# Optimization experiments

Measured on AMD Instinct MI355X. Metric: run time of the kernel, lower is better.

Reference implementation:

```python
import jax, jax.numpy as jnp
import numpy as np
from jax import lax

EPS = 1e-5  # torch BatchNorm2d default


def setup_inputs() -> dict:
    key = jax.random.key(0)
    k1, k2 = jax.random.split(key)
    x = jax.random.normal(k1, (8, 32, 28, 28), dtype=jnp.float32)
    # AdderConv.param: [out_channel, in_channel, k, k], init ~ N(0,1)
    W = jax.random.normal(k2, (64, 32, 3, 3), dtype=jnp.float32)
    # BatchNorm2d affine params at init
    gamma = jnp.ones((64,), dtype=jnp.float32)
    beta = jnp.zeros((64,), dtype=jnp.float32)
    return {"x": x, "W": W, "gamma": gamma, "beta": beta}


def _adder(patches, Wc):
    # patches: [N, K, Ho, Wo] with K = C*kh*kw (channel-major, matching torch unfold)
    # Wc: [O, K]
    # AdderNet: out[n,o,ho,wo] = -sum_k |patches[n,k,ho,wo] - Wc[o,k]|
    diff = patches[:, None, :, :, :] - Wc[None, :, :, None, None]  # [N,O,K,Ho,Wo]
    return -jnp.abs(diff).sum(axis=2)  # [N,O,Ho,Wo]


def reference(x, W, gamma, beta):
    O, C, kh, kw = W.shape
    # im2col, same layout as torch.nn.functional.unfold: feature dim = C*kh*kw
    patches = lax.conv_general_dilated_patches(
        x, (kh, kw), window_strides=(1, 1), padding=[(1, 1), (1, 1)]
    )  # [N, C*kh*kw, Ho, Wo]
    Wc = W.reshape(O, C * kh * kw)
    out = _adder(patches, Wc)  # [N, O, Ho, Wo]
    # BatchNorm2d, training mode (batch statistics, biased variance)
    mean = out.mean(axis=(0, 2, 3), keepdims=True)
    var = out.var(axis=(0, 2, 3), keepdims=True)
    y = (out - mean) * lax.rsqrt(var + EPS)
    return y * gamma[None, :, None, None] + beta[None, :, None, None]
```

## Files before the change

### kernel.cpp

```cpp
#include <hip/hip_runtime.h>

#define NB   8
#define CIN  32
#define HH   28
#define WW   28
#define OC   64
#define HWSZ (HH*WW)
#define TOTAL (NB*OC*HWSZ)
#define CNT  (NB*HWSZ)

#define TROWS 4
#define TCOLS 32
#define TSZ  (CIN*TROWS*TCOLS)

#define CPW  2
#define CHGRP 8
#define NCOPY 32

__global__ __launch_bounds__(256) void adder_stats_kernel(
    const float* __restrict__ x, const float* __restrict__ Wt,
    float* __restrict__ raw, double* __restrict__ Sbuf)
{
    __shared__ float xs[TSZ];
    const int t     = threadIdx.x;
    const int bid   = blockIdx.x;
    const int chgrp = bid & (CHGRP-1);
    const int sp    = bid >> 3;
    const int rp    = sp % 14;
    const int n     = bid / (CHGRP * 14);
    const int h0    = rp * 2;
    const int copy  = sp & (NCOPY-1);

    for (int i = t; i < TSZ; i += 256) {
        int cc  = i >> 7;
        int r   = (i >> 5) & 3;
        int col = i & 31;
        int hh  = h0 - 1 + r;
        int ww  = col - 1;
        float v = 0.0f;
        if (hh >= 0 && hh < HH && (unsigned)ww < (unsigned)WW)
            v = x[((n*CIN + cc)*HH + hh)*WW + ww];
        xs[i] = v;
    }
    __syncthreads();

    const int lane  = t & 63;
    const int g     = __builtin_amdgcn_readfirstlane(t >> 6);
    const bool valid = lane < 56;
    const int p     = valid ? lane : 0;
    const int pr    = p / WW;
    const int pw    = p % WW;
    const int o_base = chgrp*8 + g*CPW;
    const int b0    = pr*TCOLS + pw;

    float acc[CPW];
    #pragma unroll
    for (int oo = 0; oo < CPW; ++oo) acc[oo] = 0.0f;

    for (int cc = 0; cc < CIN; ++cc) {
        float xr[9];
        #pragma unroll
        for (int dr = 0; dr < 3; ++dr)
            #pragma unroll
            for (int dc = 0; dc < 3; ++dc)
                xr[dr*3+dc] = xs[(cc << 7) + b0 + (dr << 5) + dc];
        #pragma unroll
        for (int oo = 0; oo < CPW; ++oo) {
            const float* wp = Wt + ((o_base + oo)*CIN + cc)*9;
            #pragma unroll
            for (int j = 0; j < 9; ++j)
                acc[oo] += __builtin_fabsf(xr[j] - wp[j]);
        }
    }

    if (valid) {
        #pragma unroll
        for (int oo = 0; oo < CPW; ++oo)
            raw[((n*OC + o_base + oo)*HH + (h0 + pr))*WW + pw] = -acc[oo];
    }

    #pragma unroll
    for (int oo = 0; oo < CPW; ++oo) {
        float v  = valid ? -acc[oo] : 0.0f;
        float s  = v;
        float s2 = v * v;
        #pragma unroll
        for (int off = 32; off >= 1; off >>= 1) {
            s  += __shfl_xor(s,  off, 64);
            s2 += __shfl_xor(s2, off, 64);
        }
        if (lane == 0) {
            double* Sc = Sbuf + copy*128;
            atomicAdd(&Sc[     o_base + oo], (double)s);
            atomicAdd(&Sc[64 + o_base + oo], (double)s2);
        }
    }
}

__global__ __launch_bounds__(256) void bn_kernel(
    const float* __restrict__ raw, const double* __restrict__ Sbuf,
    const float* __restrict__ gamma, const float* __restrict__ beta,
    float* __restrict__ out)
{
    int i4 = blockIdx.x * 256 + threadIdx.x;
    if (i4 >= TOTAL/4) return;
    int o = (i4 / (HWSZ/4)) & (OC - 1);
    double S = 0.0, S2 = 0.0;
    #pragma unroll 8
    for (int k = 0; k < NCOPY; ++k) {
        S  += Sbuf[k*128 + o];
        S2 += Sbuf[k*128 + 64 + o];
    }
    double mean = S  * (1.0 / CNT);
    double var  = S2 * (1.0 / CNT) - mean * mean;
    double inv  = 1.0 / sqrt(var + 1e-5);
    double gs   = (double)gamma[o] * inv;
    float scl   = (float)gs;
    float sh    = (float)((double)beta[o] - mean * gs);
    float4 a = ((const float4*)raw)[i4];
    float4 v;
    v.x = a.x * scl + sh;
    v.y = a.y * scl + sh;
    v.z = a.z * scl + sh;
    v.w = a.w * scl + sh;
    ((float4*)out)[i4] = v;
}

extern "C" void kernel_launch(void* const* d_in, const int* in_sizes, int n_in,
                              void* d_out, int out_size, void* d_ws, size_t ws_size,
                              hipStream_t stream) {
    const float* x     = (const float*)d_in[0];
    const float* Wt    = (const float*)d_in[1];
    const float* gamma = (const float*)d_in[2];
    const float* beta  = (const float*)d_in[3];
    float* out = (float*)d_out;

    double* Sbuf = (double*)d_ws;
    float*  raw  = (float*)((char*)d_ws + NCOPY*128*sizeof(double));

    hipMemsetAsync(d_ws, 0, NCOPY*128*sizeof(double), stream);
    adder_stats_kernel<<<NB*14*CHGRP, 256, 0, stream>>>(x, Wt, raw, Sbuf);
    bn_kernel<<<(TOTAL/4 + 255) / 256, 256, 0, stream>>>(raw, Sbuf, gamma, beta, out);
}
```

Baseline: 83.15 us.

## Fuse adder conv and batchnorm into one cooperative kernel with grid sync

Merges the adder-conv/statistics kernel and the batchnorm kernel into a single cooperative launch. Accumulators stay in registers across a grid-wide barrier and each block normalizes its own outputs. This removes the raw intermediate buffer's global write and read, plus one kernel launch. In exchange it takes on a grid.sync over 896 blocks, which requires all blocks to be co-resident, and cooperative launch overhead. It also adds unroll pragmas to the load and channel loops.

After: 145.4 us. 1.75x slower.

```diff
diff --git a/kernel.cpp b/kernel.cpp
--- a/kernel.cpp
+++ b/kernel.cpp
@@ -1,4 +1,7 @@
 #include <hip/hip_runtime.h>
+#include <hip/hip_cooperative_groups.h>
+
+namespace cg = cooperative_groups;
 
 #define NB   8
 #define CIN  32
@@ -16,10 +19,13 @@
 #define CPW  2
 #define CHGRP 8
 #define NCOPY 32
+#define GRID (NB*14*CHGRP)
 
-__global__ __launch_bounds__(256) void adder_stats_kernel(
+__global__ __launch_bounds__(256) void fused_kernel(
     const float* __restrict__ x, const float* __restrict__ Wt,
-    float* __restrict__ raw, double* __restrict__ Sbuf)
+    double* __restrict__ Sbuf,
+    const float* __restrict__ gamma, const float* __restrict__ beta,
+    float* __restrict__ out)
 {
     __shared__ float xs[TSZ];
     const int t     = threadIdx.x;
@@ -31,6 +37,7 @@
     const int h0    = rp * 2;
     const int copy  = sp & (NCOPY-1);
 
+    #pragma unroll 4
     for (int i = t; i < TSZ; i += 256) {
         int cc  = i >> 7;
         int r   = (i >> 5) & 3;
@@ -53,10 +60,9 @@
     const int o_base = chgrp*8 + g*CPW;
     const int b0    = pr*TCOLS + pw;
 
-    float acc[CPW];
-    #pragma unroll
-    for (int oo = 0; oo < CPW; ++oo) acc[oo] = 0.0f;
+    float acc0 = 0.0f, acc1 = 0.0f;
 
+    #pragma unroll 4
     for (int cc = 0; cc < CIN; ++cc) {
         float xr[9];
         #pragma unroll
@@ -64,66 +70,63 @@
             #pragma unroll
             for (int dc = 0; dc < 3; ++dc)
                 xr[dr*3+dc] = xs[(cc << 7) + b0 + (dr << 5) + dc];
+        const float* wp0 = Wt + ((o_base    )*CIN + cc)*9;
+        const float* wp1 = Wt + ((o_base + 1)*CIN + cc)*9;
         #pragma unroll
-        for (int oo = 0; oo < CPW; ++oo) {
-            const float* wp = Wt + ((o_base + oo)*CIN + cc)*9;
-            #pragma unroll
-            for (int j = 0; j < 9; ++j)
-                acc[oo] += __builtin_fabsf(xr[j] - wp[j]);
+        for (int j = 0; j < 9; ++j) acc0 += __builtin_fabsf(xr[j] - wp0[j]);
+        #pragma unroll
+        for (int j = 0; j < 9; ++j) acc1 += __builtin_fabsf(xr[j] - wp1[j]);
+    }
+
+    {
+        float v0 = valid ? -acc0 : 0.0f;
+        float v1 = valid ? -acc1 : 0.0f;
+        float s0 = v0, q0 = v0*v0, s1 = v1, q1 = v1*v1;
+        #pragma unroll
+        for (int off = 32; off >= 1; off >>= 1) {
+            s0 += __shfl_xor(s0, off, 64);
+            q0 += __shfl_xor(q0, off, 64);
+            s1 += __shfl_xor(s1, off, 64);
+            q1 += __shfl_xor(q1, off, 64);
+        }
+        if (lane == 0) {
+            double* Sc = Sbuf + copy*128;
+            atomicAdd(&Sc[     o_base    ], (double)s0);
+            atomicAdd(&Sc[64 + o_base    ], (double)q0);
+            atomicAdd(&Sc[     o_base + 1], (double)s1);
+            atomicAdd(&Sc[64 + o_base + 1], (double)q1);
         }
     }
 
+    cg::this_grid().sync();
+
+    const int half = lane >> 5;
+    const int cidx = lane & 31;
+    const int ch   = o_base + half;
+    double Sv  = Sbuf[cidx*128 + ch];
+    double S2v = Sbuf[cidx*128 + 64 + ch];
+    #pragma unroll
+    for (int off = 16; off >= 1; off >>= 1) {
+        Sv  += __shfl_xor(Sv,  off, 64);
+        S2v += __shfl_xor(S2v, off, 64);
+    }
+    double mean = Sv  * (1.0 / CNT);
+    double var  = S2v * (1.0 / CNT) - mean * mean;
+    double gs   = (double)gamma[ch] / sqrt(var + 1e-5);
+    float scl_o = (float)gs;
+    float sh_o  = (float)((double)beta[ch] - mean * gs);
+    float scl_x = __shfl_xor(scl_o, 32, 64);
+    float sh_x  = __shfl_xor(sh_o,  32, 64);
+    float scl0 = half ? scl_x : scl_o;
+    float sh0  = half ? sh_x  : sh_o;
+    float scl1 = half ? scl_o : scl_x;
+    float sh1  = half ? sh_o  : sh_x;
+
     if (valid) {
-        #pragma unroll
-        for (int oo = 0; oo < CPW; ++oo)
-            raw[((n*OC + o_base + oo)*HH + (h0 + pr))*WW + pw] = -acc[oo];
+        const int base = (h0 + pr)*WW + pw;
+        out[(n*OC + o_base    )*HWSZ + base] = (-acc0)*scl0 + sh0;
+        out[(n*OC + o_base + 1)*HWSZ + base] = (-acc1)*scl1 + sh1;
     }
-
-    #pragma unroll
-    for (int oo = 0; oo < CPW; ++oo) {
-        float v  = valid ? -acc[oo] : 0.0f;
-        float s  = v;
-        float s2 = v * v;
-        #pragma unroll
-        for (int off = 32; off >= 1; off >>= 1) {
-            s  += __shfl_xor(s,  off, 64);
-            s2 += __shfl_xor(s2, off, 64);
-        }
-        if (lane == 0) {
-            double* Sc = Sbuf + copy*128;
-            atomicAdd(&Sc[     o_base + oo], (double)s);
-            atomicAdd(&Sc[64 + o_base + oo], (double)s2);
-        }
-    }
-}
-
-__global__ __launch_bounds__(256) void bn_kernel(
-    const float* __restrict__ raw, const double* __restrict__ Sbuf,
-    const float* __restrict__ gamma, const float* __restrict__ beta,
-    float* __restrict__ out)
-{
-    int i4 = blockIdx.x * 256 + threadIdx.x;
-    if (i4 >= TOTAL/4) return;
-    int o = (i4 / (HWSZ/4)) & (OC - 1);
-    double S = 0.0, S2 = 0.0;
-    #pragma unroll 8
-    for (int k = 0; k < NCOPY; ++k) {
-        S  += Sbuf[k*128 + o];
-        S2 += Sbuf[k*128 + 64 + o];
-    }
-    double mean = S  * (1.0 / CNT);
-    double var  = S2 * (1.0 / CNT) - mean * mean;
-    double inv  = 1.0 / sqrt(var + 1e-5);
-    double gs   = (double)gamma[o] * inv;
-    float scl   = (float)gs;
-    float sh    = (float)((double)beta[o] - mean * gs);
-    float4 a = ((const float4*)raw)[i4];
-    float4 v;
-    v.x = a.x * scl + sh;
-    v.y = a.y * scl + sh;
-    v.z = a.z * scl + sh;
-    v.w = a.w * scl + sh;
-    ((float4*)out)[i4] = v;
 }
 
 extern "C" void kernel_launch(void* const* d_in, const int* in_sizes, int n_in,
@@ -133,12 +136,13 @@
     const float* Wt    = (const float*)d_in[1];
     const float* gamma = (const float*)d_in[2];
     const float* beta  = (const float*)d_in[3];
-    float* out = (float*)d_out;
-
+    float* out  = (float*)d_out;
     double* Sbuf = (double*)d_ws;
-    float*  raw  = (float*)((char*)d_ws + NCOPY*128*sizeof(double));
 
     hipMemsetAsync(d_ws, 0, NCOPY*128*sizeof(double), stream);
-    adder_stats_kernel<<<NB*14*CHGRP, 256, 0, stream>>>(x, Wt, raw, Sbuf);
-    bn_kernel<<<(TOTAL/4 + 255) / 256, 256, 0, stream>>>(raw, Sbuf, gamma, beta, out);
+
+    void* args[] = { (void*)&x, (void*)&Wt, (void*)&Sbuf,
+                     (void*)&gamma, (void*)&beta, (void*)&out };
+    hipLaunchCooperativeKernel(reinterpret_cast<void*>(fused_kernel),
+                               dim3(GRID), dim3(256), args, 0, stream);
 }
```

## Split input-channel reduction across two waves per block and restructure BN grid

Applied to the files above, without the earlier changes.

The adder kernel now runs 512 threads per block. Pairs of waves each reduce half of the 32 input channels for the same two output channels, then combine their partial sums through shared memory before the stats reduction. This doubles the waves available to hide latency in the compute-bound loop, at the cost of an extra barrier and a shared-memory exchange. The BN kernel now uses one block per (n, o) plane, so the per-channel statistics are read once per block instead of once per thread. That plane is 196 float4s, which leaves some of the 256 threads idle.

Result: faster. 80.74 us (-2.9%).

```diff
diff --git a/kernel.cpp b/kernel.cpp
--- a/kernel.cpp
+++ b/kernel.cpp
@@ -13,25 +13,25 @@
 #define TCOLS 32
 #define TSZ  (CIN*TROWS*TCOLS)
 
-#define CPW  2
-#define CHGRP 8
 #define NCOPY 32
+#define GRID  (NB*14*8)
 
-__global__ __launch_bounds__(256) void adder_stats_kernel(
+__global__ __launch_bounds__(512) void adder_stats_kernel(
     const float* __restrict__ x, const float* __restrict__ Wt,
     float* __restrict__ raw, double* __restrict__ Sbuf)
 {
     __shared__ float xs[TSZ];
     const int t     = threadIdx.x;
     const int bid   = blockIdx.x;
-    const int chgrp = bid & (CHGRP-1);
+    const int chgrp = bid & 7;
     const int sp    = bid >> 3;
     const int rp    = sp % 14;
-    const int n     = bid / (CHGRP * 14);
+    const int n     = sp / 14;
     const int h0    = rp * 2;
     const int copy  = sp & (NCOPY-1);
 
-    for (int i = t; i < TSZ; i += 256) {
+    #pragma unroll
+    for (int i = t; i < TSZ; i += 512) {
         int cc  = i >> 7;
         int r   = (i >> 5) & 3;
         int col = i & 31;
@@ -44,55 +44,72 @@
     }
     __syncthreads();
 
-    const int lane  = t & 63;
-    const int g     = __builtin_amdgcn_readfirstlane(t >> 6);
+    const int lane   = t & 63;
+    const int w      = __builtin_amdgcn_readfirstlane(t >> 6);
+    const int khalf  = w & 1;
+    const int chpair = w >> 1;
     const bool valid = lane < 56;
-    const int p     = valid ? lane : 0;
-    const int pr    = p / WW;
-    const int pw    = p % WW;
-    const int o_base = chgrp*8 + g*CPW;
-    const int b0    = pr*TCOLS + pw;
+    const int p      = valid ? lane : 0;
+    const int pr     = p / WW;
+    const int pw     = p % WW;
+    const int o_base = chgrp*8 + chpair*2;
+    const int b0     = pr*TCOLS + pw;
+    const int c0     = khalf * 16;
 
-    float acc[CPW];
-    #pragma unroll
-    for (int oo = 0; oo < CPW; ++oo) acc[oo] = 0.0f;
+    float acc0 = 0.0f, acc1 = 0.0f;
 
-    for (int cc = 0; cc < CIN; ++cc) {
+    #pragma unroll 4
+    for (int k = 0; k < 16; ++k) {
+        const int cc = c0 + k;
         float xr[9];
         #pragma unroll
         for (int dr = 0; dr < 3; ++dr)
             #pragma unroll
             for (int dc = 0; dc < 3; ++dc)
                 xr[dr*3+dc] = xs[(cc << 7) + b0 + (dr << 5) + dc];
+        const float* wp0 = Wt + ((o_base    )*CIN + cc)*9;
+        const float* wp1 = Wt + ((o_base + 1)*CIN + cc)*9;
         #pragma unroll
-        for (int oo = 0; oo < CPW; ++oo) {
-            const float* wp = Wt + ((o_base + oo)*CIN + cc)*9;
-            #pragma unroll
-            for (int j = 0; j < 9; ++j)
-                acc[oo] += __builtin_fabsf(xr[j] - wp[j]);
-        }
+        for (int j = 0; j < 9; ++j) acc0 += __builtin_fabsf(xr[j] - wp0[j]);
+        #pragma unroll
+        for (int j = 0; j < 9; ++j) acc1 += __builtin_fabsf(xr[j] - wp1[j]);
     }
 
-    if (valid) {
-        #pragma unroll
-        for (int oo = 0; oo < CPW; ++oo)
-            raw[((n*OC + o_base + oo)*HH + (h0 + pr))*WW + pw] = -acc[oo];
+    __syncthreads();
+    if (khalf == 1 && valid) {
+        xs[chpair*112 +      lane] = acc0;
+        xs[chpair*112 + 56 + lane] = acc1;
     }
+    __syncthreads();
 
-    #pragma unroll
-    for (int oo = 0; oo < CPW; ++oo) {
-        float v  = valid ? -acc[oo] : 0.0f;
-        float s  = v;
-        float s2 = v * v;
+    if (khalf == 0) {
+        if (valid) {
+            acc0 += xs[chpair*112 +      lane];
+            acc1 += xs[chpair*112 + 56 + lane];
+        }
+        float v0 = valid ? -acc0 : 0.0f;
+        float v1 = valid ? -acc1 : 0.0f;
+
+        if (valid) {
+            const int base = (h0 + pr)*WW + pw;
+            raw[(n*OC + o_base    )*HWSZ + base] = v0;
+            raw[(n*OC + o_base + 1)*HWSZ + base] = v1;
+        }
+
+        float s0 = v0, q0 = v0*v0, s1 = v1, q1 = v1*v1;
         #pragma unroll
         for (int off = 32; off >= 1; off >>= 1) {
-            s  += __shfl_xor(s,  off, 64);
-            s2 += __shfl_xor(s2, off, 64);
+            s0 += __shfl_xor(s0, off, 64);
+            q0 += __shfl_xor(q0, off, 64);
+            s1 += __shfl_xor(s1, off, 64);
+            q1 += __shfl_xor(q1, off, 64);
         }
         if (lane == 0) {
             double* Sc = Sbuf + copy*128;
-            atomicAdd(&Sc[     o_base + oo], (double)s);
-            atomicAdd(&Sc[64 + o_base + oo], (double)s2);
+            atomicAdd(&Sc[     o_base    ], (double)s0);
+            atomicAdd(&Sc[64 + o_base    ], (double)q0);
+            atomicAdd(&Sc[     o_base + 1], (double)s1);
+            atomicAdd(&Sc[64 + o_base + 1], (double)q1);
         }
     }
 }
@@ -102,28 +119,30 @@
     const float* __restrict__ gamma, const float* __restrict__ beta,
     float* __restrict__ out)
 {
-    int i4 = blockIdx.x * 256 + threadIdx.x;
-    if (i4 >= TOTAL/4) return;
-    int o = (i4 / (HWSZ/4)) & (OC - 1);
+    const int no = blockIdx.x;
+    const int o  = no & (OC - 1);
     double S = 0.0, S2 = 0.0;
-    #pragma unroll 8
+    #pragma unroll
     for (int k = 0; k < NCOPY; ++k) {
         S  += Sbuf[k*128 + o];
         S2 += Sbuf[k*128 + 64 + o];
     }
     double mean = S  * (1.0 / CNT);
     double var  = S2 * (1.0 / CNT) - mean * mean;
-    double inv  = 1.0 / sqrt(var + 1e-5);
-    double gs   = (double)gamma[o] * inv;
-    float scl   = (float)gs;
-    float sh    = (float)((double)beta[o] - mean * gs);
-    float4 a = ((const float4*)raw)[i4];
-    float4 v;
-    v.x = a.x * scl + sh;
-    v.y = a.y * scl + sh;
-    v.z = a.z * scl + sh;
-    v.w = a.w * scl + sh;
-    ((float4*)out)[i4] = v;
+    double gs   = (double)gamma[o] / sqrt(var + 1e-5);
+    const float scl = (float)gs;
+    const float sh  = (float)((double)beta[o] - mean * gs);
+
+    const int t = threadIdx.x;
+    if (t < HWSZ/4) {
+        float4 a = ((const float4*)raw)[no*(HWSZ/4) + t];
+        float4 v;
+        v.x = a.x * scl + sh;
+        v.y = a.y * scl + sh;
+        v.z = a.z * scl + sh;
+        v.w = a.w * scl + sh;
+        ((float4*)out)[no*(HWSZ/4) + t] = v;
+    }
 }
 
 extern "C" void kernel_launch(void* const* d_in, const int* in_sizes, int n_in,
@@ -139,6 +158,6 @@
     float*  raw  = (float*)((char*)d_ws + NCOPY*128*sizeof(double));
 
     hipMemsetAsync(d_ws, 0, NCOPY*128*sizeof(double), stream);
-    adder_stats_kernel<<<NB*14*CHGRP, 256, 0, stream>>>(x, Wt, raw, Sbuf);
-    bn_kernel<<<(TOTAL/4 + 255) / 256, 256, 0, stream>>>(raw, Sbuf, gamma, beta, out);
+    adder_stats_kernel<<<GRID, 512, 0, stream>>>(x, Wt, raw, Sbuf);
+    bn_kernel<<<NB*OC, 256, 0, stream>>>(raw, Sbuf, gamma, beta, out);
 }
```
